# Optimization experiments

Measured on AMD Instinct MI355X. Metric: run time of the kernel, lower is better.

The kernel has to match this reference:

```python
import math
import jax, jax.numpy as jnp
import numpy as np

B, S, D, H, L, V = 2, 1024, 1024, 16, 6, 256
HD = D // H  # 64
PAD = 0


def setup_inputs() -> dict:
    key = jax.random.key(0)
    ks = jax.random.split(key, 22)
    s = 0.02
    f32 = jnp.float32
    inp = {
        "x": jax.random.randint(ks[0], (B, S), 0, V, dtype=jnp.int32),
        "emb": (jax.random.normal(ks[1], (V, D)) * s).astype(f32),
        "Wq": (jax.random.normal(ks[2], (L, D, D)) * s).astype(f32),
        "bq": jnp.zeros((L, D), f32),
        "Wk": (jax.random.normal(ks[3], (L, D, D)) * s).astype(f32),
        "bk": jnp.zeros((L, D), f32),
        "Wv": (jax.random.normal(ks[4], (L, D, D)) * s).astype(f32),
        "bv": jnp.zeros((L, D), f32),
        "Wo": (jax.random.normal(ks[5], (L, D, D)) * s).astype(f32),
        "bo": jnp.zeros((L, D), f32),
        "W1": (jax.random.normal(ks[6], (L, D, D // 2)) * s).astype(f32),
        "b1": jnp.zeros((L, D // 2), f32),
        "W2": (jax.random.normal(ks[7], (L, D // 2, D)) * s).astype(f32),
        "b2": jnp.zeros((L, D), f32),
        "g1": jnp.ones((L, D), f32),
        "be1": jnp.zeros((L, D), f32),
        "g2": jnp.ones((L, D), f32),
        "be2": jnp.zeros((L, D), f32),
        "E": jax.random.normal(ks[8], (L, S, HD)).astype(f32),  # relative pos embeddings, non-trainable
        "Wf": (jax.random.normal(ks[9], (D, V)) * s).astype(f32),
        "bf": jnp.zeros((V,), f32),
    }
    return inp


def _layernorm(x, g, b, eps=1e-6):
    mu = jnp.mean(x, axis=-1, keepdims=True)
    var = jnp.mean((x - mu) ** 2, axis=-1, keepdims=True)
    return (x - mu) * jax.lax.rsqrt(var + eps) * g + b


def _pos_encoding():
    # embed[p, i] = sin(p * exp(-ln(1e4)*i/D) * exp(ln(1e4)*(i%2)/D) + 0.5*pi*(i%2))
    i = jnp.arange(D, dtype=jnp.float32)
    par = jnp.mod(i, 2.0)
    rate = jnp.exp(-math.log(10000.0) * i / D) * jnp.exp(math.log(10000.0) * par / D)
    pos = jnp.arange(S, dtype=jnp.float32)
    return jnp.sin(pos[:, None] * rate[None, :] + 0.5 * math.pi * par[None, :])  # [S, D]


def _skew(QE):
    # Music Transformer skewing: pad one col on the left, reshape, drop first row.
    padded = jnp.pad(QE, ((0, 0), (0, 0), (0, 0), (1, 0)))  # [B,H,S,S+1]
    reshaped = padded.reshape(B, H, S + 1, S)
    return reshaped[:, :, 1:, :]  # [B,H,S,S]


def reference(x, emb, Wq, bq, Wk, bk, Wv, bv, Wo, bo, W1, b1, W2, b2,
              g1, be1, g2, be2, E, Wf, bf):
    pe = _pos_encoding()
    # look-ahead mask: pad positions OR strictly-future positions
    pad_mask = (x == PAD)[:, None, None, :]                      # [B,1,1,S]
    causal = jnp.triu(jnp.ones((S, S), bool), k=1)[None, None]   # [1,1,S,S]
    neg = (pad_mask | causal).astype(jnp.float32) * -1e9         # [B,1,S,S]
    # QE mask: keep qe[i, j] only where j >= S-1-i (upper-right triangle)
    idx = jnp.arange(S)
    qe_mask = (idx[None, :] >= (S - 1 - idx)[:, None]).astype(jnp.float32)

    h = emb[x] * math.sqrt(D) + pe[None]  # [B,S,D]
    scale = 1.0 / math.sqrt(HD)
    for l in range(L):
        q = (h @ Wq[l] + bq[l]).reshape(B, S, H, HD).transpose(0, 2, 1, 3)
        k = (h @ Wk[l] + bk[l]).reshape(B, S, H, HD).transpose(0, 2, 1, 3)
        v = (h @ Wv[l] + bv[l]).reshape(B, S, H, HD).transpose(0, 2, 1, 3)
        QE = jnp.einsum('bhld,md->bhlm', q, E[l]) * qe_mask
        Srel = _skew(QE)
        logits = (jnp.einsum('bhld,bhmd->bhlm', q, k) + Srel) * scale + neg
        aw = jax.nn.softmax(logits, axis=-1)
        attn = jnp.einsum('bhlm,bhmd->bhld', aw, v)
        attn = attn.transpose(0, 2, 1, 3).reshape(B, S, D)
        ao = attn @ Wo[l] + bo[l]
        o1 = _layernorm(ao, g1[l], be1[l])          # NOTE: no residual, as in source
        f = jax.nn.relu(o1 @ W1[l] + b1[l]) @ W2[l] + b2[l]
        h = _layernorm(f, g2[l], be2[l])
    return h @ Wf + bf  # [B,S,V]
```

## Files before the change

kernel.cpp:

```cpp
#include <hip/hip_runtime.h>
#include <hip/hip_bf16.h>


typedef __attribute__((ext_vector_type(8))) short  s8_t;
typedef __attribute__((ext_vector_type(4))) short  s4_t;
typedef __attribute__((ext_vector_type(8))) __bf16 bf8_t;
typedef __attribute__((ext_vector_type(4))) float  f4v;

static __device__ __forceinline__ short f2bf(float f) {
  union { float f; unsigned u; } a; a.f = f;
  unsigned u = a.u;
  u += 0x7fffu + ((u >> 16) & 1u);
  return (short)(u >> 16);
}
static __device__ __forceinline__ float bf2f(short s) {
  union { float f; unsigned u; } a;
  a.u = ((unsigned)(unsigned short)s) << 16;
  return a.f;
}
static __device__ __forceinline__ f4v mfma16(s8_t a, s8_t b, f4v c) {
  return __builtin_amdgcn_mfma_f32_16x16x32_bf16(
      __builtin_bit_cast(bf8_t, a), __builtin_bit_cast(bf8_t, b), c, 0, 0, 0);
}
static __device__ __forceinline__ void gld16(const short* g, short* l) {
  __builtin_amdgcn_global_load_lds(
      (const __attribute__((address_space(1))) void*)g,
      (__attribute__((address_space(3))) void*)l, 16, 0, 0);
}

static __device__ const int IT_TAB[40] = {
  15,15,15,15, 14,14,14,14, 13,13,13,13, 12,12,12,12,
  11,11,11, 10,10,10, 9,9,9, 8,8,8,
  7,7, 6,6, 5,5, 4,4, 3, 2, 1, 0};
static __device__ const int CW_TAB[40] = {
  0,1,2,3, 0,1,2,3, 0,1,2,3, 0,1,2,3,
  0,1,2, 0,1,2, 0,1,2, 0,1,2,
  0,1, 0,1, 0,1, 0,1, 0, 0, 0, 0};

__global__ void transpose_bf16(const float* __restrict__ in, short* __restrict__ out,
                               int R, int C, long outBS, int outRowOff) {
  __shared__ float tile[32][33];
  const long zi = (long)blockIdx.z * R * C;
  out += (long)blockIdx.z * outBS + (long)outRowOff * R;
  const int c0 = blockIdx.x * 32, r0 = blockIdx.y * 32;
  const int tx = threadIdx.x, ty = threadIdx.y;
#pragma unroll
  for (int i = 0; i < 4; i++)
    tile[ty + i * 8][tx] = in[zi + (long)(r0 + ty + i * 8) * C + c0 + tx];
  __syncthreads();
#pragma unroll
  for (int i = 0; i < 4; i++)
    out[(long)(c0 + ty + i * 8) * R + r0 + tx] = f2bf(tile[tx][ty + i * 8]);
}

__global__ __launch_bounds__(256) void cvt_bf16(const float* __restrict__ in,
                                                short* __restrict__ out) {
  const long i = ((long)blockIdx.x * 256 + threadIdx.x) * 4;
  const float4 t = *(const float4*)(in + i);
  s4_t o = {f2bf(t.x), f2bf(t.y), f2bf(t.z), f2bf(t.w)};
  *(s4_t*)(out + i) = o;
}

__global__ void qkv_bias_kernel(const float* __restrict__ bq, const float* __restrict__ bk,
                                const float* __restrict__ bv, float* __restrict__ out) {
  const int idx = blockIdx.x * 256 + threadIdx.x;
  const int l = idx / 3072, n = idx % 3072;
  float v = (n < 1024) ? bq[l * 1024 + n]
          : (n < 2048) ? bk[l * 1024 + n - 1024]
                       : bv[l * 1024 + n - 2048];
  out[idx] = v;
}

__global__ void fnp_kernel(const int* __restrict__ x, int* __restrict__ fnp) {
  const int b = blockIdx.x, lane = threadIdx.x;
  int first = 1024;
  for (int j0 = 0; j0 < 1024; j0 += 64) {
    unsigned long long m = __ballot(x[b * 1024 + j0 + lane] != 0);
    if (m) { first = j0 + __ffsll(m) - 1; break; }
  }
  if (lane == 0) fnp[b] = first;
}

__global__ __launch_bounds__(256) void embed_kernel(const int* __restrict__ x,
                                                    const float* __restrict__ emb,
                                                    short* __restrict__ h) {
  const int row = blockIdx.x;
  const int s = row & 1023;
  const int xv = x[row];
  const int c = threadIdx.x << 2;
  const float4 e = *(const float4*)(emb + (long)xv * 1024 + c);
  const float ev[4] = {e.x, e.y, e.z, e.w};
  s4_t o;
#pragma unroll
  for (int i = 0; i < 4; i++) {
    const int d = c + i;
    const float par = (float)(d & 1);
    const float rate = expf(-9.210340371976184f * (float)d / 1024.0f) *
                       expf(9.210340371976184f * par / 1024.0f);
    const float pe = sinf((float)s * rate + 1.5707963267948966f * par);
    o[i] = f2bf(ev[i] * 32.0f + pe);
  }
  *(s4_t*)(h + (long)row * 1024 + c) = o;
}

__global__ __launch_bounds__(256) void ln_kernel(const short* __restrict__ in,
                                                 short* __restrict__ out,
                                                 const float* __restrict__ g,
                                                 const float* __restrict__ be) {
  __shared__ float red[4];
  __shared__ float red2[4];
  const int row = blockIdx.x;
  const int tid = threadIdx.x;
  const int c = tid << 2;
  const s4_t xv = *(const s4_t*)(in + (long)row * 1024 + c);
  const float x0 = bf2f(xv[0]), x1 = bf2f(xv[1]), x2 = bf2f(xv[2]), x3 = bf2f(xv[3]);
  float s = x0 + x1 + x2 + x3;
#pragma unroll
  for (int off = 1; off < 64; off <<= 1) s += __shfl_xor(s, off);
  const int wave = tid >> 6, lane = tid & 63;
  if (lane == 0) red[wave] = s;
  __syncthreads();
  const float mu = (red[0] + red[1] + red[2] + red[3]) * (1.0f / 1024.0f);
  const float d0 = x0 - mu, d1 = x1 - mu, d2 = x2 - mu, d3 = x3 - mu;
  float q = d0 * d0 + d1 * d1 + d2 * d2 + d3 * d3;
#pragma unroll
  for (int off = 1; off < 64; off <<= 1) q += __shfl_xor(q, off);
  if (lane == 0) red2[wave] = q;
  __syncthreads();
  const float var = (red2[0] + red2[1] + red2[2] + red2[3]) * (1.0f / 1024.0f);
  const float rs = rsqrtf(var + 1e-6f);
  const float4 gv = *(const float4*)(g + c);
  const float4 bv = *(const float4*)(be + c);
  s4_t o = {f2bf(d0 * rs * gv.x + bv.x), f2bf(d1 * rs * gv.y + bv.y),
            f2bf(d2 * rs * gv.z + bv.z), f2bf(d3 * rs * gv.w + bv.w)};
  *(s4_t*)(out + (long)row * 1024 + c) = o;
}

template <int BM, int BN, int WR, int WC, int OUT_BF16, int RELU, int SKEW = 0>
__global__ __launch_bounds__(256) void gemm_lds(
    const short* __restrict__ A, const short* __restrict__ BT,
    void* __restrict__ Cv, const float* __restrict__ biasp,
    int K, int lda, int ldb, int ldc,
    int batH, long sA1, long sA2, long sBT, long sC, int qeSkip) {
  constexpr int AR = BM / 64, BR = BN / 64;
  constexpr int FI = BM / WR / 16, FJ = BN / WC / 16;
  __shared__ short As[BM * 32];
  __shared__ short Bs[BN * 32];
  const int bm = blockIdx.y * BM, bn = blockIdx.x * BN;
  if (qeSkip && (bm + bn + BM + BN - 2 < 1023)) return;
  const int tid = threadIdx.x;
  const int z = blockIdx.z;
  const int wave = tid >> 6, lane = tid & 63;
  const int quad = lane >> 4, l16 = lane & 15;
  const int wr = wave / WC, wc = wave % WC;
  const int wm = wr * (BM / WR), wn = wc * (BN / WC);

  const short* Az = A + (long)(z / batH) * sA1 + (long)(z % batH) * sA2;
  const short* Bz = BT + (long)z * sBT;
  const short* Ag = Az + (long)(bm + wave * 16 + (lane >> 2)) * lda + ((lane & 3) << 3);
  const short* Bg = Bz + (long)(bn + wave * 16 + (lane >> 2)) * ldb + ((lane & 3) << 3);

  f4v acc[FI][FJ];
#pragma unroll
  for (int i = 0; i < FI; i++)
#pragma unroll
    for (int j = 0; j < FJ; j++) {
      f4v zz = {0.f, 0.f, 0.f, 0.f};
      acc[i][j] = zz;
    }

  for (int k0 = 0; k0 < K; k0 += 32) {
#pragma unroll
    for (int r = 0; r < AR; r++)
      gld16(Ag + (long)r * 64 * lda + k0, As + r * 2048 + wave * 512);
#pragma unroll
    for (int r = 0; r < BR; r++)
      gld16(Bg + (long)r * 64 * ldb + k0, Bs + r * 2048 + wave * 512);
    __syncthreads();
    s8_t af[FI], bfr[FJ];
#pragma unroll
    for (int t = 0; t < FI; t++)
      af[t] = *(const s8_t*)&As[(wm + t * 16 + l16) * 32 + quad * 8];
#pragma unroll
    for (int t = 0; t < FJ; t++)
      bfr[t] = *(const s8_t*)&Bs[(wn + t * 16 + l16) * 32 + quad * 8];
#pragma unroll
    for (int ti = 0; ti < FI; ti++)
#pragma unroll
      for (int tj = 0; tj < FJ; tj++)
        acc[ti][tj] = mfma16(af[ti], bfr[tj], acc[ti][tj]);
    __syncthreads();
  }

  char* Cb = (char*)Cv + (long)z * sC * (OUT_BF16 ? 2 : 4);
#pragma unroll
  for (int ti = 0; ti < FI; ti++) {
#pragma unroll
    for (int tj = 0; tj < FJ; tj++) {
      const int n = bn + wn + tj * 16 + l16;
      const float bval = (!SKEW && biasp) ? biasp[n] : 0.f;
#pragma unroll
      for (int r = 0; r < 4; r++) {
        const int m = bm + wm + ti * 16 + quad * 4 + r;
        if (SKEW) {
          const int j = n - 1023 + m;
          if (j >= 0)
            ((short*)Cb)[(long)m * ldc + j] = f2bf(acc[ti][tj][r] * 0.125f);
        } else {
          float vv = acc[ti][tj][r] + bval;
          if (RELU) vv = fmaxf(vv, 0.f);
          if (OUT_BF16) ((short*)Cb)[(long)m * ldc + n] = f2bf(vv);
          else          ((float*)Cb)[(long)m * ldc + n] = vv;
        }
      }
    }
  }
}

__global__ __launch_bounds__(256) void attn_main(
    const short* __restrict__ qkv, const short* __restrict__ SM,
    const int* __restrict__ xids,
    float* __restrict__ PO, float* __restrict__ PM, float* __restrict__ PL) {
  __shared__ short Ks2[8][128][8];
  __shared__ short Vt[64][136];
  __shared__ short Ps[4][16][136];
  __shared__ float kneg[128];

  const int bh = blockIdx.x, b = bh >> 4, hh = bh & 15;
  const int itile = IT_TAB[blockIdx.y], cw = CW_TAB[blockIdx.y];
  const int tid = threadIdx.x;
  const int wave = tid >> 6, lane = tid & 63, quad = lane >> 4, l16 = lane & 15;
  const int i0 = itile * 64 + wave * 16;

  s8_t aq[2];
  {
    const short* qp = qkv + ((long)(b * 1024 + i0 + l16)) * 3072 + hh * 64 + quad * 8;
    aq[0] = *(const s8_t*)qp;
    aq[1] = *(const s8_t*)(qp + 32);
  }

  f4v o[4];
#pragma unroll
  for (int nt = 0; nt < 4; nt++) { f4v zz = {0.f, 0.f, 0.f, 0.f}; o[nt] = zz; }
  float m_run[4] = {-INFINITY, -INFINITY, -INFINITY, -INFINITY};
  float l_run[4] = {0.f, 0.f, 0.f, 0.f};

  const int half = wave >> 1;
  const int krow = ((wave & 1) << 6) + lane;
  const short* kgl = qkv + ((long)b * 1024 + lane) * 3072 + 1024 + hh * 64 + wave * 8;
  const short* vgw = qkv + ((long)(b * 1024 + krow)) * 3072 + 2048 + hh * 64 + half * 32;

  const int irow = i0 + quad * 4;
  const short* smr[4];
#pragma unroll
  for (int r = 0; r < 4; r++)
    smr[r] = SM + ((long)bh * 1024 + irow + r) * 1024;

  const int jBeg = cw * 256;
  const int jEnd = min(cw * 256 + 256, itile * 64 + 64);

  for (int j0 = jBeg; j0 < jEnd; j0 += 128) {
    const long jrow = (long)j0 * 3072;
    gld16(kgl + jrow, &Ks2[wave][0][0]);
    gld16(kgl + jrow + (long)64 * 3072, &Ks2[wave][64][0]);
    gld16(kgl + jrow + 32, &Ks2[wave + 4][0][0]);
    gld16(kgl + jrow + (long)64 * 3072 + 32, &Ks2[wave + 4][64][0]);
    {
      const short* vrow = vgw + jrow;
      const s8_t v0 = *(const s8_t*)(vrow);
      const s8_t v1 = *(const s8_t*)(vrow + 8);
      const s8_t v2 = *(const s8_t*)(vrow + 16);
      const s8_t v3 = *(const s8_t*)(vrow + 24);
#pragma unroll
      for (int t = 0; t < 8; t++) {
        Vt[half * 32 + t][krow] = v0[t];
        Vt[half * 32 + 8 + t][krow] = v1[t];
        Vt[half * 32 + 16 + t][krow] = v2[t];
        Vt[half * 32 + 24 + t][krow] = v3[t];
      }
    }
    if (tid < 128) kneg[tid] = (xids[b * 1024 + j0 + tid] == 0) ? -1e9f : 0.0f;
    __syncthreads();

    float p[8][4];
#pragma unroll
    for (int jt = 0; jt < 8; jt++) {
      const s8_t k0f = *(const s8_t*)&Ks2[quad][jt * 16 + l16][0];
      const s8_t k1f = *(const s8_t*)&Ks2[4 + quad][jt * 16 + l16][0];
      f4v zz = {0.f, 0.f, 0.f, 0.f};
      zz = mfma16(aq[0], k0f, zz);
      zz = mfma16(aq[1], k1f, zz);
      const int j = j0 + jt * 16 + l16;
      const float kn = kneg[jt * 16 + l16];
#pragma unroll
      for (int r = 0; r < 4; r++) {
        const float add = bf2f(smr[r][j]) + kn;
        p[jt][r] = zz[r] * 0.125f + ((j <= irow + r) ? add : -1e9f);
      }
    }

    float alpha[4];
#pragma unroll
    for (int r = 0; r < 4; r++) {
      float mx = p[0][r];
#pragma unroll
      for (int jt = 1; jt < 8; jt++) mx = fmaxf(mx, p[jt][r]);
      mx = fmaxf(mx, __shfl_xor(mx, 1));
      mx = fmaxf(mx, __shfl_xor(mx, 2));
      mx = fmaxf(mx, __shfl_xor(mx, 4));
      mx = fmaxf(mx, __shfl_xor(mx, 8));
      const float mnew = fmaxf(m_run[r], mx);
      alpha[r] = expf(m_run[r] - mnew);
      float ps = 0.f;
#pragma unroll
      for (int jt = 0; jt < 8; jt++) {
        p[jt][r] = expf(p[jt][r] - mnew);
        ps += p[jt][r];
      }
      ps += __shfl_xor(ps, 1);
      ps += __shfl_xor(ps, 2);
      ps += __shfl_xor(ps, 4);
      ps += __shfl_xor(ps, 8);
      l_run[r] = l_run[r] * alpha[r] + ps;
      m_run[r] = mnew;
    }

#pragma unroll
    for (int jt = 0; jt < 8; jt++)
#pragma unroll
      for (int r = 0; r < 4; r++)
        Ps[wave][quad * 4 + r][jt * 16 + l16] = f2bf(p[jt][r]);
#pragma unroll
    for (int nt = 0; nt < 4; nt++)
#pragma unroll
      for (int r = 0; r < 4; r++)
        o[nt][r] *= alpha[r];

#pragma unroll
    for (int ks4 = 0; ks4 < 4; ks4++) {
      const s8_t ap = *(const s8_t*)&Ps[wave][l16][ks4 * 32 + quad * 8];
#pragma unroll
      for (int nt = 0; nt < 4; nt++) {
        const s8_t vf = *(const s8_t*)&Vt[nt * 16 + l16][ks4 * 32 + quad * 8];
        o[nt] = mfma16(ap, vf, o[nt]);
      }
    }
    __syncthreads();
  }

  const long part = (long)(bh * 16 + itile) * 4 + cw;
  float* po = PO + part * 4096;
#pragma unroll
  for (int nt = 0; nt < 4; nt++) {
#pragma unroll
    for (int r = 0; r < 4; r++) {
      const int row = wave * 16 + quad * 4 + r;
      po[row * 64 + nt * 16 + l16] = o[nt][r];
    }
  }
  if (l16 == 0) {
#pragma unroll
    for (int r = 0; r < 4; r++) {
      const int row = wave * 16 + quad * 4 + r;
      PM[part * 64 + row] = m_run[r];
      PL[part * 64 + row] = l_run[r];
    }
  }
}

__global__ __launch_bounds__(256) void attn_combine(
    const float* __restrict__ PO, const float* __restrict__ PM,
    const float* __restrict__ PL, short* __restrict__ outb) {
  const int id = blockIdx.x;
  const int bh = id >> 4, itile = id & 15;
  const int b = bh >> 4, hh = bh & 15;
  const int nc = (itile >> 2) + 1;
  const int row = threadIdx.x >> 2, seg = (threadIdx.x & 3) << 4;
  const long base = (long)id * 4;

  float mv[4];
  float M = -INFINITY;
  for (int c = 0; c < nc; c++) {
    mv[c] = PM[(base + c) * 64 + row];
    M = fmaxf(M, mv[c]);
  }
  f4v acc[4];
#pragma unroll
  for (int t = 0; t < 4; t++) { f4v zz = {0.f, 0.f, 0.f, 0.f}; acc[t] = zz; }
  float l = 0.f;
  for (int c = 0; c < nc; c++) {
    const float w = expf(mv[c] - M);
    l += w * PL[(base + c) * 64 + row];
    const float* po = PO + (base + c) * 4096 + row * 64 + seg;
#pragma unroll
    for (int t = 0; t < 4; t++) {
      const f4v v = *(const f4v*)(po + t * 4);
      acc[t] += w * v;
    }
  }
  const float inv = 1.0f / l;
  const int i = itile * 64 + row;
  short* op = outb + ((long)(b * 1024 + i)) * 1024 + hh * 64 + seg;
#pragma unroll
  for (int t = 0; t < 4; t++) {
    s4_t o = {f2bf(acc[t][0] * inv), f2bf(acc[t][1] * inv),
              f2bf(acc[t][2] * inv), f2bf(acc[t][3] * inv)};
    *(s4_t*)(op + t * 4) = o;
  }
}

__global__ __launch_bounds__(256) void attn_fallback(
    const short* __restrict__ qkv, const short* __restrict__ SM,
    const int* __restrict__ fnp, short* __restrict__ outb) {
  const int bh = blockIdx.x, b = bh >> 4, hh = bh & 15;
  const int itile = blockIdx.y;
  const int fb = fnp[b];
  if (fb <= itile * 64) return;

  __shared__ short Ks[64][72];
  __shared__ short Vt[64][72];
  __shared__ short Ps[4][16][72];

  const int tid = threadIdx.x;
  const int wave = tid >> 6, lane = tid & 63, quad = lane >> 4, l16 = lane & 15;
  const int i0 = itile * 64 + wave * 16;

  s8_t aq[2];
  {
    const short* qp = qkv + ((long)(b * 1024 + i0 + l16)) * 3072 + hh * 64 + quad * 8;
    aq[0] = *(const s8_t*)qp;
    aq[1] = *(const s8_t*)(qp + 32);
  }
  f4v o[4];
#pragma unroll
  for (int nt = 0; nt < 4; nt++) { f4v zz = {0.f, 0.f, 0.f, 0.f}; o[nt] = zz; }
  float m_run[4] = {-INFINITY, -INFINITY, -INFINITY, -INFINITY};
  float l_run[4] = {0.f, 0.f, 0.f, 0.f};

  const int jr = tid >> 2, c0 = (tid & 3) << 4;
  const short* kp0 = qkv + ((long)(b * 1024 + jr)) * 3072 + 1024 + hh * 64 + c0;
  const short* vp0 = kp0 + 1024;

  for (int j0 = 0; j0 < 1024; j0 += 64) {
    const long joff = (long)j0 * 3072;
    *(s8_t*)&Ks[jr][c0] = *(const s8_t*)(kp0 + joff);
    *(s8_t*)&Ks[jr][c0 + 8] = *(const s8_t*)(kp0 + joff + 8);
    const s8_t v0 = *(const s8_t*)(vp0 + joff);
    const s8_t v1 = *(const s8_t*)(vp0 + joff + 8);
#pragma unroll
    for (int t = 0; t < 8; t++) {
      Vt[c0 + t][jr] = v0[t];
      Vt[c0 + 8 + t][jr] = v1[t];
    }
    __syncthreads();

    f4v sc[4];
#pragma unroll
    for (int nt = 0; nt < 4; nt++) {
      const s8_t k0f = *(const s8_t*)&Ks[nt * 16 + l16][quad * 8];
      const s8_t k1f = *(const s8_t*)&Ks[nt * 16 + l16][32 + quad * 8];
      f4v zz = {0.f, 0.f, 0.f, 0.f};
      zz = mfma16(aq[0], k0f, zz);
      zz = mfma16(aq[1], k1f, zz);
      sc[nt] = zz;
    }
    float p[4][4];
    const int irow = i0 + quad * 4;
#pragma unroll
    for (int nt = 0; nt < 4; nt++) {
      const int j = j0 + nt * 16 + l16;
#pragma unroll
      for (int r = 0; r < 4; r++) {
        const int i = irow + r;
        const float smv = bf2f(SM[((long)bh * 1024 + i) * 1024 + j]);
        p[nt][r] = sc[nt][r] * 0.125f + ((j <= i) ? smv : 0.f);
      }
    }
    float alpha[4];
#pragma unroll
    for (int r = 0; r < 4; r++) {
      float mx = fmaxf(fmaxf(p[0][r], p[1][r]), fmaxf(p[2][r], p[3][r]));
      mx = fmaxf(mx, __shfl_xor(mx, 1));
      mx = fmaxf(mx, __shfl_xor(mx, 2));
      mx = fmaxf(mx, __shfl_xor(mx, 4));
      mx = fmaxf(mx, __shfl_xor(mx, 8));
      const float mnew = fmaxf(m_run[r], mx);
      alpha[r] = expf(m_run[r] - mnew);
      float ps = 0.f;
#pragma unroll
      for (int nt = 0; nt < 4; nt++) {
        p[nt][r] = expf(p[nt][r] - mnew);
        ps += p[nt][r];
      }
      ps += __shfl_xor(ps, 1);
      ps += __shfl_xor(ps, 2);
      ps += __shfl_xor(ps, 4);
      ps += __shfl_xor(ps, 8);
      l_run[r] = l_run[r] * alpha[r] + ps;
      m_run[r] = mnew;
    }
#pragma unroll
    for (int nt = 0; nt < 4; nt++) {
#pragma unroll
      for (int r = 0; r < 4; r++) {
        Ps[wave][quad * 4 + r][nt * 16 + l16] = f2bf(p[nt][r]);
        o[nt][r] *= alpha[r];
      }
    }
#pragma unroll
    for (int ks = 0; ks < 2; ks++) {
      const s8_t ap = *(const s8_t*)&Ps[wave][l16][ks * 32 + quad * 8];
#pragma unroll
      for (int nt = 0; nt < 4; nt++) {
        const s8_t vf = *(const s8_t*)&Vt[nt * 16 + l16][ks * 32 + quad * 8];
        o[nt] = mfma16(ap, vf, o[nt]);
      }
    }
    __syncthreads();
  }

#pragma unroll
  for (int nt = 0; nt < 4; nt++) {
#pragma unroll
    for (int r = 0; r < 4; r++) {
      const int i = i0 + quad * 4 + r;
      if (i < fb)
        outb[((long)(b * 1024 + i)) * 1024 + hh * 64 + nt * 16 + l16] =
            f2bf(o[nt][r] / l_run[r]);
    }
  }
}

extern "C" void kernel_launch(void* const* d_in, const int* in_sizes, int n_in,
                              void* d_out, int out_size, void* d_ws, size_t ws_size,
                              hipStream_t stream) {
  const int*   x   = (const int*)d_in[0];
  const float* emb = (const float*)d_in[1];
  const float* Wq  = (const float*)d_in[2];
  const float* bq  = (const float*)d_in[3];
  const float* Wk  = (const float*)d_in[4];
  const float* bk  = (const float*)d_in[5];
  const float* Wv  = (const float*)d_in[6];
  const float* bv  = (const float*)d_in[7];
  const float* Wo  = (const float*)d_in[8];
  const float* bo  = (const float*)d_in[9];
  const float* W1  = (const float*)d_in[10];
  const float* b1  = (const float*)d_in[11];
  const float* W2  = (const float*)d_in[12];
  const float* b2  = (const float*)d_in[13];
  const float* g1  = (const float*)d_in[14];
  const float* be1 = (const float*)d_in[15];
  const float* g2  = (const float*)d_in[16];
  const float* be2 = (const float*)d_in[17];
  const float* E   = (const float*)d_in[18];
  const float* Wf  = (const float*)d_in[19];
  const float* bfv = (const float*)d_in[20];

  char* p = (char*)d_ws;
  auto alloc = [&](size_t bytes) {
    char* r = p;
    p += (bytes + 255) & ~(size_t)255;
    return r;
  };
  short* h    = (short*)alloc(2048ull * 1024 * 2);
  short* qkv  = (short*)alloc(2048ull * 3072 * 2);
  short* attn = (short*)alloc(2048ull * 1024 * 2);
  short* tmp  = (short*)alloc(2048ull * 1024 * 2);
  short* mid  = (short*)alloc(2048ull * 512 * 2);
  short* SMb  = (short*)alloc(32ull * 1024 * 1024 * 2);
  short* qkvT = (short*)alloc(6ull * 3072 * 1024 * 2);
  short* WoT  = (short*)alloc(6ull * 1024 * 1024 * 2);
  short* W1T  = (short*)alloc(6ull * 512 * 1024 * 2);
  short* W2T  = (short*)alloc(6ull * 1024 * 512 * 2);
  short* WfT  = (short*)alloc(256ull * 1024 * 2);
  short* Ebf  = (short*)alloc(6ull * 1024 * 64 * 2);
  float* qkvB = (float*)alloc(6ull * 3072 * 4);
  int*   fnp  = (int*)alloc(256);
  float* PO   = (float*)alloc(2048ull * 4096 * 4);
  float* PM   = (float*)alloc(2048ull * 64 * 4);
  float* PL   = (float*)alloc(2048ull * 64 * 4);

  const dim3 tb(32, 8);
  transpose_bf16<<<dim3(32, 32, 6), tb, 0, stream>>>(Wq, qkvT, 1024, 1024, 3072 * 1024, 0);
  transpose_bf16<<<dim3(32, 32, 6), tb, 0, stream>>>(Wk, qkvT, 1024, 1024, 3072 * 1024, 1024);
  transpose_bf16<<<dim3(32, 32, 6), tb, 0, stream>>>(Wv, qkvT, 1024, 1024, 3072 * 1024, 2048);
  transpose_bf16<<<dim3(32, 32, 6), tb, 0, stream>>>(Wo, WoT, 1024, 1024, 1024 * 1024, 0);
  transpose_bf16<<<dim3(16, 32, 6), tb, 0, stream>>>(W1, W1T, 1024, 512, 512 * 1024, 0);
  transpose_bf16<<<dim3(32, 16, 6), tb, 0, stream>>>(W2, W2T, 512, 1024, 1024 * 512, 0);
  transpose_bf16<<<dim3(8, 32, 1), tb, 0, stream>>>(Wf, WfT, 1024, 256, 256 * 1024, 0);
  cvt_bf16<<<384, 256, 0, stream>>>(E, Ebf);
  qkv_bias_kernel<<<72, 256, 0, stream>>>(bq, bk, bv, qkvB);
  fnp_kernel<<<2, 64, 0, stream>>>(x, fnp);
  embed_kernel<<<2048, 256, 0, stream>>>(x, emb, h);

  for (int l = 0; l < 6; l++) {
    const long wOff = (long)l * 1024 * 1024;
    const long w12Off = (long)l * 512 * 1024;
    gemm_lds<128, 128, 2, 2, 1, 0><<<dim3(24, 16, 1), 256, 0, stream>>>(
        h, qkvT + (long)l * 3072 * 1024, qkv, qkvB + l * 3072,
        1024, 1024, 1024, 3072, 1, 0, 0, 0, 0, 0);
    gemm_lds<128, 128, 2, 2, 1, 0, 1><<<dim3(8, 8, 32), 256, 0, stream>>>(
        qkv, Ebf + (long)l * 1024 * 64, SMb, nullptr,
        64, 3072, 64, 1024, 16, (long)1024 * 3072, 64, 0, (long)1024 * 1024, 1);
    attn_main<<<dim3(32, 40), 256, 0, stream>>>(qkv, SMb, x, PO, PM, PL);
    attn_combine<<<512, 256, 0, stream>>>(PO, PM, PL, attn);
    attn_fallback<<<dim3(32, 16), 256, 0, stream>>>(qkv, SMb, fnp, attn);
    gemm_lds<64, 64, 2, 2, 1, 0><<<dim3(16, 32, 1), 256, 0, stream>>>(
        attn, WoT + wOff, tmp, bo + l * 1024, 1024, 1024, 1024, 1024, 1, 0, 0, 0, 0, 0);
    ln_kernel<<<2048, 256, 0, stream>>>(tmp, tmp, g1 + l * 1024, be1 + l * 1024);
    gemm_lds<64, 64, 2, 2, 1, 1><<<dim3(8, 32, 1), 256, 0, stream>>>(
        tmp, W1T + w12Off, mid, b1 + l * 512, 1024, 1024, 1024, 512, 1, 0, 0, 0, 0, 0);
    gemm_lds<64, 64, 2, 2, 1, 0><<<dim3(16, 32, 1), 256, 0, stream>>>(
        mid, W2T + w12Off, h, b2 + l * 1024, 512, 512, 512, 1024, 1, 0, 0, 0, 0, 0);
    ln_kernel<<<2048, 256, 0, stream>>>(h, h, g2 + l * 1024, be2 + l * 1024);
  }
  gemm_lds<64, 64, 2, 2, 0, 0><<<dim3(4, 32, 1), 256, 0, stream>>>(
      h, WfT, (float*)d_out, bfv, 1024, 1024, 1024, 256, 1, 0, 0, 0, 0, 0);
}
```

Baseline: 1.075 ms.

## Fuse relative-position QE computation into attention and merge fallback and prep kernels

The relative-position QE GEMM, which wrote a 64 MB skewed bf16 matrix, is removed. Each attention block now computes the needed diagonal band of q·E on the fly with MFMA into shared memory and reads the skewed values from there. The separate fallback attention kernel for rows before the first non-pad token is folded into attn_main as extra grid rows. The last i-tile group writes its output directly rather than going through combine. Setup work is merged into two prep kernels to reduce launches. This trades the global-memory round trip for extra MFMA work and shared-memory use inside the attention kernel.

```diff
diff --git a/kernel.cpp b/kernel.cpp
--- a/kernel.cpp
+++ b/kernel.cpp
@@ -37,70 +37,91 @@
   0,1,2, 0,1,2, 0,1,2, 0,1,2,
   0,1, 0,1, 0,1, 0,1, 0, 0, 0, 0};
 
-__global__ void transpose_bf16(const float* __restrict__ in, short* __restrict__ out,
-                               int R, int C, long outBS, int outRowOff) {
+__global__ void prep_weights(
+    const float* __restrict__ Wq, const float* __restrict__ Wk,
+    const float* __restrict__ Wv, const float* __restrict__ Wo,
+    const float* __restrict__ W1, const float* __restrict__ W2,
+    const float* __restrict__ Wf,
+    short* __restrict__ qkvT, short* __restrict__ WoT, short* __restrict__ W1T,
+    short* __restrict__ W2T, short* __restrict__ WfT) {
   __shared__ float tile[32][33];
-  const long zi = (long)blockIdx.z * R * C;
-  out += (long)blockIdx.z * outBS + (long)outRowOff * R;
-  const int c0 = blockIdx.x * 32, r0 = blockIdx.y * 32;
+  int z = blockIdx.x;
+  const float* in; short* out; int R, C; long outBS; int rowOff = 0;
+  if (z < 18432) {
+    R = 1024; C = 1024; outBS = (long)3072 * 1024; out = qkvT;
+    if (z < 6144)       { in = Wq; }
+    else if (z < 12288) { in = Wk; rowOff = 1024; z -= 6144; }
+    else                { in = Wv; rowOff = 2048; z -= 12288; }
+  } else if (z < 24576) { in = Wo; out = WoT; R = 1024; C = 1024; outBS = (long)1024 * 1024; z -= 18432; }
+  else if (z < 27648)   { in = W1; out = W1T; R = 1024; C = 512;  outBS = (long)512 * 1024;  z -= 24576; }
+  else if (z < 30720)   { in = W2; out = W2T; R = 512;  C = 1024; outBS = (long)1024 * 512;  z -= 27648; }
+  else                  { in = Wf; out = WfT; R = 1024; C = 256;  outBS = 0;                 z -= 30720; }
+  const int nx = C >> 5, ny = R >> 5;
+  const int per = nx * ny;
+  const int l = z / per, rem = z % per;
+  const int cx = rem % nx, cy = rem / nx;
+  in += (long)l * R * C;
+  out += (long)l * outBS + (long)rowOff * R;
+  const int c0 = cx * 32, r0 = cy * 32;
   const int tx = threadIdx.x, ty = threadIdx.y;
 #pragma unroll
   for (int i = 0; i < 4; i++)
-    tile[ty + i * 8][tx] = in[zi + (long)(r0 + ty + i * 8) * C + c0 + tx];
+    tile[ty + i * 8][tx] = in[(long)(r0 + ty + i * 8) * C + c0 + tx];
   __syncthreads();
 #pragma unroll
   for (int i = 0; i < 4; i++)
     out[(long)(c0 + ty + i * 8) * R + r0 + tx] = f2bf(tile[tx][ty + i * 8]);
 }
 
-__global__ __launch_bounds__(256) void cvt_bf16(const float* __restrict__ in,
-                                                short* __restrict__ out) {
-  const long i = ((long)blockIdx.x * 256 + threadIdx.x) * 4;
-  const float4 t = *(const float4*)(in + i);
-  s4_t o = {f2bf(t.x), f2bf(t.y), f2bf(t.z), f2bf(t.w)};
-  *(s4_t*)(out + i) = o;
-}
-
-__global__ void qkv_bias_kernel(const float* __restrict__ bq, const float* __restrict__ bk,
-                                const float* __restrict__ bv, float* __restrict__ out) {
-  const int idx = blockIdx.x * 256 + threadIdx.x;
-  const int l = idx / 3072, n = idx % 3072;
-  float v = (n < 1024) ? bq[l * 1024 + n]
-          : (n < 2048) ? bk[l * 1024 + n - 1024]
-                       : bv[l * 1024 + n - 2048];
-  out[idx] = v;
-}
-
-__global__ void fnp_kernel(const int* __restrict__ x, int* __restrict__ fnp) {
-  const int b = blockIdx.x, lane = threadIdx.x;
-  int first = 1024;
-  for (int j0 = 0; j0 < 1024; j0 += 64) {
-    unsigned long long m = __ballot(x[b * 1024 + j0 + lane] != 0);
-    if (m) { first = j0 + __ffsll(m) - 1; break; }
-  }
-  if (lane == 0) fnp[b] = first;
-}
-
-__global__ __launch_bounds__(256) void embed_kernel(const int* __restrict__ x,
-                                                    const float* __restrict__ emb,
-                                                    short* __restrict__ h) {
-  const int row = blockIdx.x;
-  const int s = row & 1023;
-  const int xv = x[row];
-  const int c = threadIdx.x << 2;
-  const float4 e = *(const float4*)(emb + (long)xv * 1024 + c);
-  const float ev[4] = {e.x, e.y, e.z, e.w};
-  s4_t o;
-#pragma unroll
-  for (int i = 0; i < 4; i++) {
-    const int d = c + i;
-    const float par = (float)(d & 1);
-    const float rate = expf(-9.210340371976184f * (float)d / 1024.0f) *
-                       expf(9.210340371976184f * par / 1024.0f);
-    const float pe = sinf((float)s * rate + 1.5707963267948966f * par);
-    o[i] = f2bf(ev[i] * 32.0f + pe);
-  }
-  *(s4_t*)(h + (long)row * 1024 + c) = o;
+__global__ __launch_bounds__(256) void prep_misc(
+    const int* __restrict__ x, const float* __restrict__ emb,
+    const float* __restrict__ E,
+    const float* __restrict__ bq, const float* __restrict__ bk,
+    const float* __restrict__ bv,
+    short* __restrict__ h, short* __restrict__ Ebf,
+    float* __restrict__ qkvB, int* __restrict__ fnp) {
+  const int z = blockIdx.x;
+  const int tid = threadIdx.x;
+  if (z < 2048) {
+    const int s = z & 1023;
+    const int xv = x[z];
+    const int c = tid << 2;
+    const float4 e = *(const float4*)(emb + (long)xv * 1024 + c);
+    const float ev[4] = {e.x, e.y, e.z, e.w};
+    s4_t o;
+#pragma unroll
+    for (int i = 0; i < 4; i++) {
+      const int d = c + i;
+      const float par = (float)(d & 1);
+      const float rate = expf(-9.210340371976184f * (float)d / 1024.0f) *
+                         expf(9.210340371976184f * par / 1024.0f);
+      const float pe = sinf((float)s * rate + 1.5707963267948966f * par);
+      o[i] = f2bf(ev[i] * 32.0f + pe);
+    }
+    *(s4_t*)(h + (long)z * 1024 + c) = o;
+  } else if (z < 2432) {
+    const long i = ((long)(z - 2048) * 256 + tid) * 4;
+    const float4 t = *(const float4*)(E + i);
+    s4_t o = {f2bf(t.x), f2bf(t.y), f2bf(t.z), f2bf(t.w)};
+    *(s4_t*)(Ebf + i) = o;
+  } else if (z < 2504) {
+    const int idx = (z - 2432) * 256 + tid;
+    const int l = idx / 3072, n = idx % 3072;
+    float v = (n < 1024) ? bq[l * 1024 + n]
+            : (n < 2048) ? bk[l * 1024 + n - 1024]
+                         : bv[l * 1024 + n - 2048];
+    qkvB[idx] = v;
+  } else {
+    if (tid < 64) {
+      const int b = z - 2504;
+      int first = 1024;
+      for (int j0 = 0; j0 < 1024; j0 += 64) {
+        unsigned long long m = __ballot(x[b * 1024 + j0 + tid] != 0);
+        if (m) { first = j0 + __ffsll(m) - 1; break; }
+      }
+      if (tid == 0) fnp[b] = first;
+    }
+  }
 }
 
 __global__ __launch_bounds__(256) void ln_kernel(const short* __restrict__ in,
@@ -136,29 +157,24 @@
   *(s4_t*)(out + (long)row * 1024 + c) = o;
 }
 
-template <int BM, int BN, int WR, int WC, int OUT_BF16, int RELU, int SKEW = 0>
+template <int BM, int BN, int WR, int WC, int OUT_BF16, int RELU>
 __global__ __launch_bounds__(256) void gemm_lds(
     const short* __restrict__ A, const short* __restrict__ BT,
     void* __restrict__ Cv, const float* __restrict__ biasp,
-    int K, int lda, int ldb, int ldc,
-    int batH, long sA1, long sA2, long sBT, long sC, int qeSkip) {
+    int K, int lda, int ldb, int ldc) {
   constexpr int AR = BM / 64, BR = BN / 64;
   constexpr int FI = BM / WR / 16, FJ = BN / WC / 16;
   __shared__ short As[BM * 32];
   __shared__ short Bs[BN * 32];
   const int bm = blockIdx.y * BM, bn = blockIdx.x * BN;
-  if (qeSkip && (bm + bn + BM + BN - 2 < 1023)) return;
   const int tid = threadIdx.x;
-  const int z = blockIdx.z;
   const int wave = tid >> 6, lane = tid & 63;
   const int quad = lane >> 4, l16 = lane & 15;
   const int wr = wave / WC, wc = wave % WC;
   const int wm = wr * (BM / WR), wn = wc * (BN / WC);
 
-  const short* Az = A + (long)(z / batH) * sA1 + (long)(z % batH) * sA2;
-  const short* Bz = BT + (long)z * sBT;
-  const short* Ag = Az + (long)(bm + wave * 16 + (lane >> 2)) * lda + ((lane & 3) << 3);
-  const short* Bg = Bz + (long)(bn + wave * 16 + (lane >> 2)) * ldb + ((lane & 3) << 3);
+  const short* Ag = A + (long)(bm + wave * 16 + (lane >> 2)) * lda + ((lane & 3) << 3);
+  const short* Bg = BT + (long)(bn + wave * 16 + (lane >> 2)) * ldb + ((lane & 3) << 3);
 
   f4v acc[FI][FJ];
 #pragma unroll
@@ -192,45 +208,46 @@
     __syncthreads();
   }
 
-  char* Cb = (char*)Cv + (long)z * sC * (OUT_BF16 ? 2 : 4);
 #pragma unroll
   for (int ti = 0; ti < FI; ti++) {
 #pragma unroll
     for (int tj = 0; tj < FJ; tj++) {
       const int n = bn + wn + tj * 16 + l16;
-      const float bval = (!SKEW && biasp) ? biasp[n] : 0.f;
+      const float bval = biasp ? biasp[n] : 0.f;
 #pragma unroll
       for (int r = 0; r < 4; r++) {
         const int m = bm + wm + ti * 16 + quad * 4 + r;
-        if (SKEW) {
-          const int j = n - 1023 + m;
-          if (j >= 0)
-            ((short*)Cb)[(long)m * ldc + j] = f2bf(acc[ti][tj][r] * 0.125f);
-        } else {
-          float vv = acc[ti][tj][r] + bval;
-          if (RELU) vv = fmaxf(vv, 0.f);
-          if (OUT_BF16) ((short*)Cb)[(long)m * ldc + n] = f2bf(vv);
-          else          ((float*)Cb)[(long)m * ldc + n] = vv;
-        }
+        float vv = acc[ti][tj][r] + bval;
+        if (RELU) vv = fmaxf(vv, 0.f);
+        if (OUT_BF16) ((short*)Cv)[(long)m * ldc + n] = f2bf(vv);
+        else          ((float*)Cv)[(long)m * ldc + n] = vv;
       }
     }
   }
 }
 
 __global__ __launch_bounds__(256) void attn_main(
-    const short* __restrict__ qkv, const short* __restrict__ SM,
-    const int* __restrict__ xids,
-    float* __restrict__ PO, float* __restrict__ PM, float* __restrict__ PL) {
+    const short* __restrict__ qkv, const short* __restrict__ Eb,
+    const int* __restrict__ xids, const int* __restrict__ fnp,
+    float* __restrict__ PO, float* __restrict__ PM, float* __restrict__ PL,
+    short* __restrict__ outb) {
   __shared__ short Ks2[8][128][8];
   __shared__ short Vt[64][136];
-  __shared__ short Ps[4][16][136];
+  __shared__ short Gs[4][16][152];
   __shared__ float kneg[128];
 
   const int bh = blockIdx.x, b = bh >> 4, hh = bh & 15;
-  const int itile = IT_TAB[blockIdx.y], cw = CW_TAB[blockIdx.y];
+  const int yy = blockIdx.y;
+  const bool fbp = (yy >= 40);
+  const int itile = fbp ? (yy - 40) : IT_TAB[yy];
+  const int cw = fbp ? 0 : CW_TAB[yy];
+  const int fb = fnp[b];
+  const int i0g = itile * 64;
+  if (fbp && fb <= i0g) return;
+
   const int tid = threadIdx.x;
   const int wave = tid >> 6, lane = tid & 63, quad = lane >> 4, l16 = lane & 15;
-  const int i0 = itile * 64 + wave * 16;
+  const int i0 = i0g + wave * 16;
 
   s8_t aq[2];
   {
@@ -247,26 +264,23 @@
 
   const int half = wave >> 1;
   const int krow = ((wave & 1) << 6) + lane;
-  const short* kgl = qkv + ((long)b * 1024 + lane) * 3072 + 1024 + hh * 64 + wave * 8;
-  const short* vgw = qkv + ((long)(b * 1024 + krow)) * 3072 + 2048 + hh * 64 + half * 32;
-
-  const int irow = i0 + quad * 4;
-  const short* smr[4];
-#pragma unroll
-  for (int r = 0; r < 4; r++)
-    smr[r] = SM + ((long)bh * 1024 + irow + r) * 1024;
-
-  const int jBeg = cw * 256;
-  const int jEnd = min(cw * 256 + 256, itile * 64 + 64);
+  const short* kbase = qkv + (long)b * 1024 * 3072 + 1024 + hh * 64 + wave * 8;
+  const short* vbase = qkv + (long)b * 1024 * 3072 + 2048 + hh * 64 + half * 32;
+  short* gs = &Gs[wave][0][0];
+
+  const int jBeg = fbp ? 0 : cw * 256;
+  const int jEnd = fbp ? 1024 : min(cw * 256 + 256, i0g + 64);
 
   for (int j0 = jBeg; j0 < jEnd; j0 += 128) {
-    const long jrow = (long)j0 * 3072;
-    gld16(kgl + jrow, &Ks2[wave][0][0]);
-    gld16(kgl + jrow + (long)64 * 3072, &Ks2[wave][64][0]);
-    gld16(kgl + jrow + 32, &Ks2[wave + 4][0][0]);
-    gld16(kgl + jrow + (long)64 * 3072 + 32, &Ks2[wave + 4][64][0]);
     {
-      const short* vrow = vgw + jrow;
+      const long k1 = min(j0 + lane, 1023);
+      const long k2 = min(j0 + 64 + lane, 1023);
+      gld16(kbase + k1 * 3072, &Ks2[wave][0][0]);
+      gld16(kbase + k2 * 3072, &Ks2[wave][64][0]);
+      gld16(kbase + k1 * 3072 + 32, &Ks2[wave + 4][0][0]);
+      gld16(kbase + k2 * 3072 + 32, &Ks2[wave + 4][64][0]);
+      const long kv = min(j0 + krow, 1023);
+      const short* vrow = vbase + kv * 3072;
       const s8_t v0 = *(const s8_t*)(vrow);
       const s8_t v1 = *(const s8_t*)(vrow + 8);
       const s8_t v2 = *(const s8_t*)(vrow + 16);
@@ -279,10 +293,28 @@
         Vt[half * 32 + 24 + t][krow] = v3[t];
       }
     }
-    if (tid < 128) kneg[tid] = (xids[b * 1024 + j0 + tid] == 0) ? -1e9f : 0.0f;
+    if (tid < 128) kneg[tid] = (xids[b * 1024 + min(j0 + tid, 1023)] == 0) ? -1e9f : 0.0f;
+
+    {
+      const int mW = 1008 - i0g - wave * 16 + j0;
+#pragma unroll
+      for (int t = 0; t < 9; t++) {
+        const int m = min(mW + t * 16 + l16, 1023);
+        const short* ep = Eb + m * 64 + quad * 8;
+        const s8_t eb0 = *(const s8_t*)ep;
+        const s8_t eb1 = *(const s8_t*)(ep + 32);
+        f4v g = {0.f, 0.f, 0.f, 0.f};
+        g = mfma16(aq[0], eb0, g);
+        g = mfma16(aq[1], eb1, g);
+#pragma unroll
+        for (int r = 0; r < 4; r++)
+          gs[(quad * 4 + r) * 152 + t * 16 + l16] = f2bf(g[r]);
+      }
+    }
     __syncthreads();
 
     float p[8][4];
+    const int irow = i0 + quad * 4;
 #pragma unroll
     for (int jt = 0; jt < 8; jt++) {
       const s8_t k0f = *(const s8_t*)&Ks2[quad][jt * 16 + l16][0];
@@ -294,8 +326,12 @@
       const float kn = kneg[jt * 16 + l16];
 #pragma unroll
       for (int r = 0; r < 4; r++) {
-        const float add = bf2f(smr[r][j]) + kn;
-        p[jt][r] = zz[r] * 0.125f + ((j <= irow + r) ? add : -1e9f);
+        const int rr = quad * 4 + r;
+        const float smv = bf2f(gs[rr * 151 + 15 + jt * 16 + l16]);
+        const bool causal = (j <= irow + r);
+        const float srel = causal ? smv : 0.f;
+        const float kk = fbp ? 0.f : (causal ? kn : -1e9f);
+        p[jt][r] = (zz[r] + srel) * 0.125f + kk;
       }
     }
 
@@ -329,7 +365,7 @@
     for (int jt = 0; jt < 8; jt++)
 #pragma unroll
       for (int r = 0; r < 4; r++)
-        Ps[wave][quad * 4 + r][jt * 16 + l16] = f2bf(p[jt][r]);
+        gs[(quad * 4 + r) * 152 + jt * 16 + l16] = f2bf(p[jt][r]);
 #pragma unroll
     for (int nt = 0; nt < 4; nt++)
 #pragma unroll
@@ -338,7 +374,7 @@
 
 #pragma unroll
     for (int ks4 = 0; ks4 < 4; ks4++) {
-      const s8_t ap = *(const s8_t*)&Ps[wave][l16][ks4 * 32 + quad * 8];
+      const s8_t ap = *(const s8_t*)&gs[l16 * 152 + ks4 * 32 + quad * 8];
 #pragma unroll
       for (int nt = 0; nt < 4; nt++) {
         const s8_t vf = *(const s8_t*)&Vt[nt * 16 + l16][ks4 * 32 + quad * 8];
@@ -348,35 +384,59 @@
     __syncthreads();
   }
 
-  const long part = (long)(bh * 16 + itile) * 4 + cw;
-  float* po = PO + part * 4096;
-#pragma unroll
-  for (int nt = 0; nt < 4; nt++) {
-#pragma unroll
-    for (int r = 0; r < 4; r++) {
-      const int row = wave * 16 + quad * 4 + r;
-      po[row * 64 + nt * 16 + l16] = o[nt][r];
-    }
-  }
-  if (l16 == 0) {
-#pragma unroll
-    for (int r = 0; r < 4; r++) {
-      const int row = wave * 16 + quad * 4 + r;
-      PM[part * 64 + row] = m_run[r];
-      PL[part * 64 + row] = l_run[r];
+  if (fbp) {
+#pragma unroll
+    for (int nt = 0; nt < 4; nt++)
+#pragma unroll
+      for (int r = 0; r < 4; r++) {
+        const int i = i0 + quad * 4 + r;
+        if (i < fb)
+          outb[((long)(b * 1024 + i)) * 1024 + hh * 64 + nt * 16 + l16] =
+              f2bf(o[nt][r] / l_run[r]);
+      }
+  } else if (yy >= 36) {
+#pragma unroll
+    for (int nt = 0; nt < 4; nt++)
+#pragma unroll
+      for (int r = 0; r < 4; r++) {
+        const int i = i0 + quad * 4 + r;
+        if (i >= fb)
+          outb[((long)(b * 1024 + i)) * 1024 + hh * 64 + nt * 16 + l16] =
+              f2bf(o[nt][r] / l_run[r]);
+      }
+  } else {
+    const long part = (long)(bh * 16 + itile) * 4 + cw;
+    float* po = PO + part * 4096;
+#pragma unroll
+    for (int nt = 0; nt < 4; nt++)
+#pragma unroll
+      for (int r = 0; r < 4; r++) {
+        const int row = wave * 16 + quad * 4 + r;
+        po[row * 64 + nt * 16 + l16] = o[nt][r];
+      }
+    if (l16 == 0) {
+#pragma unroll
+      for (int r = 0; r < 4; r++) {
+        const int row = wave * 16 + quad * 4 + r;
+        PM[part * 64 + row] = m_run[r];
+        PL[part * 64 + row] = l_run[r];
+      }
     }
   }
 }
 
 __global__ __launch_bounds__(256) void attn_combine(
     const float* __restrict__ PO, const float* __restrict__ PM,
-    const float* __restrict__ PL, short* __restrict__ outb) {
+    const float* __restrict__ PL, const int* __restrict__ fnp,
+    short* __restrict__ outb) {
   const int id = blockIdx.x;
-  const int bh = id >> 4, itile = id & 15;
+  const int bh = id / 12, itile = 4 + id % 12;
   const int b = bh >> 4, hh = bh & 15;
   const int nc = (itile >> 2) + 1;
   const int row = threadIdx.x >> 2, seg = (threadIdx.x & 3) << 4;
-  const long base = (long)id * 4;
+  const long base = (long)(bh * 16 + itile) * 4;
+  const int i = itile * 64 + row;
+  if (i < fnp[b]) return;
 
   float mv[4];
   float M = -INFINITY;
@@ -399,135 +459,12 @@
     }
   }
   const float inv = 1.0f / l;
-  const int i = itile * 64 + row;
   short* op = outb + ((long)(b * 1024 + i)) * 1024 + hh * 64 + seg;
 #pragma unroll
   for (int t = 0; t < 4; t++) {
     s4_t o = {f2bf(acc[t][0] * inv), f2bf(acc[t][1] * inv),
               f2bf(acc[t][2] * inv), f2bf(acc[t][3] * inv)};
     *(s4_t*)(op + t * 4) = o;
-  }
-}
-
-__global__ __launch_bounds__(256) void attn_fallback(
-    const short* __restrict__ qkv, const short* __restrict__ SM,
-    const int* __restrict__ fnp, short* __restrict__ outb) {
-  const int bh = blockIdx.x, b = bh >> 4, hh = bh & 15;
-  const int itile = blockIdx.y;
-  const int fb = fnp[b];
-  if (fb <= itile * 64) return;
-
-  __shared__ short Ks[64][72];
-  __shared__ short Vt[64][72];
-  __shared__ short Ps[4][16][72];
-
-  const int tid = threadIdx.x;
-  const int wave = tid >> 6, lane = tid & 63, quad = lane >> 4, l16 = lane & 15;
-  const int i0 = itile * 64 + wave * 16;
-
-  s8_t aq[2];
-  {
-    const short* qp = qkv + ((long)(b * 1024 + i0 + l16)) * 3072 + hh * 64 + quad * 8;
-    aq[0] = *(const s8_t*)qp;
-    aq[1] = *(const s8_t*)(qp + 32);
-  }
-  f4v o[4];
-#pragma unroll
-  for (int nt = 0; nt < 4; nt++) { f4v zz = {0.f, 0.f, 0.f, 0.f}; o[nt] = zz; }
-  float m_run[4] = {-INFINITY, -INFINITY, -INFINITY, -INFINITY};
-  float l_run[4] = {0.f, 0.f, 0.f, 0.f};
-
-  const int jr = tid >> 2, c0 = (tid & 3) << 4;
-  const short* kp0 = qkv + ((long)(b * 1024 + jr)) * 3072 + 1024 + hh * 64 + c0;
-  const short* vp0 = kp0 + 1024;
-
-  for (int j0 = 0; j0 < 1024; j0 += 64) {
-    const long joff = (long)j0 * 3072;
-    *(s8_t*)&Ks[jr][c0] = *(const s8_t*)(kp0 + joff);
-    *(s8_t*)&Ks[jr][c0 + 8] = *(const s8_t*)(kp0 + joff + 8);
-    const s8_t v0 = *(const s8_t*)(vp0 + joff);
-    const s8_t v1 = *(const s8_t*)(vp0 + joff + 8);
-#pragma unroll
-    for (int t = 0; t < 8; t++) {
-      Vt[c0 + t][jr] = v0[t];
-      Vt[c0 + 8 + t][jr] = v1[t];
-    }
-    __syncthreads();
-
-    f4v sc[4];
-#pragma unroll
-    for (int nt = 0; nt < 4; nt++) {
-      const s8_t k0f = *(const s8_t*)&Ks[nt * 16 + l16][quad * 8];
-      const s8_t k1f = *(const s8_t*)&Ks[nt * 16 + l16][32 + quad * 8];
-      f4v zz = {0.f, 0.f, 0.f, 0.f};
-      zz = mfma16(aq[0], k0f, zz);
-      zz = mfma16(aq[1], k1f, zz);
-      sc[nt] = zz;
-    }
-    float p[4][4];
-    const int irow = i0 + quad * 4;
-#pragma unroll
-    for (int nt = 0; nt < 4; nt++) {
-      const int j = j0 + nt * 16 + l16;
-#pragma unroll
-      for (int r = 0; r < 4; r++) {
-        const int i = irow + r;
-        const float smv = bf2f(SM[((long)bh * 1024 + i) * 1024 + j]);
-        p[nt][r] = sc[nt][r] * 0.125f + ((j <= i) ? smv : 0.f);
-      }
-    }
-    float alpha[4];
-#pragma unroll
-    for (int r = 0; r < 4; r++) {
-      float mx = fmaxf(fmaxf(p[0][r], p[1][r]), fmaxf(p[2][r], p[3][r]));
-      mx = fmaxf(mx, __shfl_xor(mx, 1));
-      mx = fmaxf(mx, __shfl_xor(mx, 2));
-      mx = fmaxf(mx, __shfl_xor(mx, 4));
-      mx = fmaxf(mx, __shfl_xor(mx, 8));
-      const float mnew = fmaxf(m_run[r], mx);
-      alpha[r] = expf(m_run[r] - mnew);
-      float ps = 0.f;
-#pragma unroll
-      for (int nt = 0; nt < 4; nt++) {
-        p[nt][r] = expf(p[nt][r] - mnew);
-        ps += p[nt][r];
-      }
-      ps += __shfl_xor(ps, 1);
-      ps += __shfl_xor(ps, 2);
-      ps += __shfl_xor(ps, 4);
-      ps += __shfl_xor(ps, 8);
-      l_run[r] = l_run[r] * alpha[r] + ps;
-      m_run[r] = mnew;
-    }
-#pragma unroll
-    for (int nt = 0; nt < 4; nt++) {
-#pragma unroll
-      for (int r = 0; r < 4; r++) {
-        Ps[wave][quad * 4 + r][nt * 16 + l16] = f2bf(p[nt][r]);
-        o[nt][r] *= alpha[r];
-      }
-    }
-#pragma unroll
-    for (int ks = 0; ks < 2; ks++) {
-      const s8_t ap = *(const s8_t*)&Ps[wave][l16][ks * 32 + quad * 8];
-#pragma unroll
-      for (int nt = 0; nt < 4; nt++) {
-        const s8_t vf = *(const s8_t*)&Vt[nt * 16 + l16][ks * 32 + quad * 8];
-        o[nt] = mfma16(ap, vf, o[nt]);
-      }
-    }
-    __syncthreads();
-  }
-
-#pragma unroll
-  for (int nt = 0; nt < 4; nt++) {
-#pragma unroll
-    for (int r = 0; r < 4; r++) {
-      const int i = i0 + quad * 4 + r;
-      if (i < fb)
-        outb[((long)(b * 1024 + i)) * 1024 + hh * 64 + nt * 16 + l16] =
-            f2bf(o[nt][r] / l_run[r]);
-    }
   }
 }
 
@@ -567,7 +504,6 @@
   short* attn = (short*)alloc(2048ull * 1024 * 2);
   short* tmp  = (short*)alloc(2048ull * 1024 * 2);
   short* mid  = (short*)alloc(2048ull * 512 * 2);
-  short* SMb  = (short*)alloc(32ull * 1024 * 1024 * 2);
   short* qkvT = (short*)alloc(6ull * 3072 * 1024 * 2);
   short* WoT  = (short*)alloc(6ull * 1024 * 1024 * 2);
   short* W1T  = (short*)alloc(6ull * 512 * 1024 * 2);
@@ -580,40 +516,27 @@
   float* PM   = (float*)alloc(2048ull * 64 * 4);
   float* PL   = (float*)alloc(2048ull * 64 * 4);
 
-  const dim3 tb(32, 8);
-  transpose_bf16<<<dim3(32, 32, 6), tb, 0, stream>>>(Wq, qkvT, 1024, 1024, 3072 * 1024, 0);
-  transpose_bf16<<<dim3(32, 32, 6), tb, 0, stream>>>(Wk, qkvT, 1024, 1024, 3072 * 1024, 1024);
-  transpose_bf16<<<dim3(32, 32, 6), tb, 0, stream>>>(Wv, qkvT, 1024, 1024, 3072 * 1024, 2048);
-  transpose_bf16<<<dim3(32, 32, 6), tb, 0, stream>>>(Wo, WoT, 1024, 1024, 1024 * 1024, 0);
-  transpose_bf16<<<dim3(16, 32, 6), tb, 0, stream>>>(W1, W1T, 1024, 512, 512 * 1024, 0);
-  transpose_bf16<<<dim3(32, 16, 6), tb, 0, stream>>>(W2, W2T, 512, 1024, 1024 * 512, 0);
-  transpose_bf16<<<dim3(8, 32, 1), tb, 0, stream>>>(Wf, WfT, 1024, 256, 256 * 1024, 0);
-  cvt_bf16<<<384, 256, 0, stream>>>(E, Ebf);
-  qkv_bias_kernel<<<72, 256, 0, stream>>>(bq, bk, bv, qkvB);
-  fnp_kernel<<<2, 64, 0, stream>>>(x, fnp);
-  embed_kernel<<<2048, 256, 0, stream>>>(x, emb, h);
+  prep_weights<<<30976, dim3(32, 8), 0, stream>>>(
+      Wq, Wk, Wv, Wo, W1, W2, Wf, qkvT, WoT, W1T, W2T, WfT);
+  prep_misc<<<2506, 256, 0, stream>>>(x, emb, E, bq, bk, bv, h, Ebf, qkvB, fnp);
 
   for (int l = 0; l < 6; l++) {
     const long wOff = (long)l * 1024 * 1024;
     const long w12Off = (long)l * 512 * 1024;
-    gemm_lds<128, 128, 2, 2, 1, 0><<<dim3(24, 16, 1), 256, 0, stream>>>(
-        h, qkvT + (long)l * 3072 * 1024, qkv, qkvB + l * 3072,
-        1024, 1024, 1024, 3072, 1, 0, 0, 0, 0, 0);
-    gemm_lds<128, 128, 2, 2, 1, 0, 1><<<dim3(8, 8, 32), 256, 0, stream>>>(
-        qkv, Ebf + (long)l * 1024 * 64, SMb, nullptr,
-        64, 3072, 64, 1024, 16, (long)1024 * 3072, 64, 0, (long)1024 * 1024, 1);
-    attn_main<<<dim3(32, 40), 256, 0, stream>>>(qkv, SMb, x, PO, PM, PL);
-    attn_combine<<<512, 256, 0, stream>>>(PO, PM, PL, attn);
-    attn_fallback<<<dim3(32, 16), 256, 0, stream>>>(qkv, SMb, fnp, attn);
-    gemm_lds<64, 64, 2, 2, 1, 0><<<dim3(16, 32, 1), 256, 0, stream>>>(
-        attn, WoT + wOff, tmp, bo + l * 1024, 1024, 1024, 1024, 1024, 1, 0, 0, 0, 0, 0);
+    gemm_lds<128, 128, 2, 2, 1, 0><<<dim3(24, 16), 256, 0, stream>>>(
+        h, qkvT + (long)l * 3072 * 1024, qkv, qkvB + l * 3072, 1024, 1024, 1024, 3072);
+    attn_main<<<dim3(32, 56), 256, 0, stream>>>(
+        qkv, Ebf + (long)l * 1024 * 64, x, fnp, PO, PM, PL, attn);
+    attn_combine<<<384, 256, 0, stream>>>(PO, PM, PL, fnp, attn);
+    gemm_lds<64, 64, 2, 2, 1, 0><<<dim3(16, 32), 256, 0, stream>>>(
+        attn, WoT + wOff, tmp, bo + l * 1024, 1024, 1024, 1024, 1024);
     ln_kernel<<<2048, 256, 0, stream>>>(tmp, tmp, g1 + l * 1024, be1 + l * 1024);
-    gemm_lds<64, 64, 2, 2, 1, 1><<<dim3(8, 32, 1), 256, 0, stream>>>(
-        tmp, W1T + w12Off, mid, b1 + l * 512, 1024, 1024, 1024, 512, 1, 0, 0, 0, 0, 0);
-    gemm_lds<64, 64, 2, 2, 1, 0><<<dim3(16, 32, 1), 256, 0, stream>>>(
-        mid, W2T + w12Off, h, b2 + l * 1024, 512, 512, 512, 1024, 1, 0, 0, 0, 0, 0);
+    gemm_lds<64, 64, 2, 2, 1, 1><<<dim3(8, 32), 256, 0, stream>>>(
+        tmp, W1T + w12Off, mid, b1 + l * 512, 1024, 1024, 1024, 512);
+    gemm_lds<64, 64, 2, 2, 1, 0><<<dim3(16, 32), 256, 0, stream>>>(
+        mid, W2T + w12Off, h, b2 + l * 1024, 512, 512, 512, 1024);
     ln_kernel<<<2048, 256, 0, stream>>>(h, h, g2 + l * 1024, be2 + l * 1024);
   }
-  gemm_lds<64, 64, 2, 2, 0, 0><<<dim3(4, 32, 1), 256, 0, stream>>>(
-      h, WfT, (float*)d_out, bfv, 1024, 1024, 1024, 256, 1, 0, 0, 0, 0, 0);
-}
+  gemm_lds<64, 64, 2, 2, 0, 0><<<dim3(4, 32), 256, 0, stream>>>(
+      h, WfT, (float*)d_out, bfv, 1024, 1024, 1024, 256);
+}
```

Measured after the change: 978.8 us. 9.0% less time.
